# Kernel optimization log

Hardware: AMD Instinct MI355X
Metric: run time of the kernel (lower is better)

Reference implementation:

```python
import jax, jax.numpy as jnp
import numpy as np

N, L, D = 16, 128, 128
H, C = 8, 16
EPS = 1e-5


def setup_inputs() -> dict:
    key = jax.random.key(0)
    ks = jax.random.split(key, 10)
    s = 0.02
    return {
        "z": jax.random.normal(ks[0], (N, L, L, D), dtype=jnp.float32),
        "ln_w": jnp.ones((D,), jnp.float32),
        "ln_b": jnp.zeros((D,), jnp.float32),
        "Wq": jax.random.normal(ks[1], (D, H * C), jnp.float32) * s,
        "Wk": jax.random.normal(ks[2], (D, H * C), jnp.float32) * s,
        "Wv": jax.random.normal(ks[3], (D, H * C), jnp.float32) * s,
        "Wg": jax.random.normal(ks[4], (D, H * C), jnp.float32) * s,
        "bg": jnp.zeros((H * C,), jnp.float32),
        "Wo": jax.random.normal(ks[5], (H * C, D), jnp.float32) * s,
        "bo": jnp.zeros((D,), jnp.float32),
    }


def reference(z, ln_w, ln_b, Wq, Wk, Wv, Wg, bg, Wo, bo):
    n, l, _, d = z.shape
    # LayerNorm over channel dim
    mu = jnp.mean(z, axis=-1, keepdims=True)
    var = jnp.var(z, axis=-1, keepdims=True)
    zn = (z - mu) * jax.lax.rsqrt(var + EPS) * ln_w + ln_b
    # projections -> (N, L, L, H, C)
    q = (zn @ Wq).reshape(n, l, l, H, C)
    k = (zn @ Wk).reshape(n, l, l, H, C)
    v = (zn @ Wv).reshape(n, l, l, H, C)
    g = jax.nn.sigmoid(zn @ Wg + bg).reshape(n, l, l, H, C)
    # attention over the sample axis N, per pair position (a,b) and head h
    att = jnp.einsum('iabhc,jabhc->ijabh', q, k) * (1.0 / np.sqrt(C))
    att = jax.nn.softmax(att, axis=1)
    o = jnp.einsum('ijabh,jabhc->iabhc', att, v) * g
    out = o.reshape(n, l, l, H * C) @ Wo + bo
    return out
```

## Files before the change

### kernel.cpp

```cpp
#include <hip/hip_runtime.h>
#include <hip/hip_bf16.h>


typedef short bf16x8 __attribute__((ext_vector_type(8)));
typedef float f32x4 __attribute__((ext_vector_type(4)));

#define MFMA16x32(A, B, C) __builtin_amdgcn_mfma_f32_16x16x32_bf16((A), (B), (C), 0, 0, 0)

__device__ __forceinline__ unsigned short f2bf(float f) {
    unsigned int u = __float_as_uint(f);
    u += 0x7fffu + ((u >> 16) & 1u);
    return (unsigned short)(u >> 16);
}

template <int CTRL>
__device__ __forceinline__ float dpp_mov16(float x) {
    return __int_as_float(__builtin_amdgcn_update_dpp(
        0, __float_as_int(x), CTRL, 0xf, 0xf, true));
}
__device__ __forceinline__ float red16_sum(float x) {
    x += dpp_mov16<0xB1>(x);
    x += dpp_mov16<0x4E>(x);
    x += dpp_mov16<0x141>(x);
    x += dpp_mov16<0x140>(x);
    return x;
}
__device__ __forceinline__ float red16_max(float x) {
    x = fmaxf(x, dpp_mov16<0xB1>(x));
    x = fmaxf(x, dpp_mov16<0x4E>(x));
    x = fmaxf(x, dpp_mov16<0x141>(x));
    x = fmaxf(x, dpp_mov16<0x140>(x));
    return x;
}

static constexpr int  DD     = 128;
static constexpr int  NPOS   = 128 * 128;
static constexpr long ZSTR   = (long)NPOS * DD;
static constexpr int  ZN_STR = 136;
static constexpr int  SB_STR = 56;

__launch_bounds__(256, 2)
__global__ void ssattn_fused(const float* __restrict__ z,
                             const float* __restrict__ ln_w,
                             const float* __restrict__ ln_b,
                             const float* __restrict__ Wq,
                             const float* __restrict__ Wk,
                             const float* __restrict__ Wv,
                             const float* __restrict__ Wg,
                             const float* __restrict__ bg,
                             const float* __restrict__ Wo,
                             const float* __restrict__ bo,
                             float* __restrict__ out)
{
    __shared__ __align__(16) unsigned short zn_s[16 * ZN_STR];
    __shared__ __align__(16) unsigned short ob_s[16 * ZN_STR];
    __shared__ __align__(16) unsigned short qb_s[4][16 * SB_STR];
    __shared__ __align__(16) unsigned short kq_s[4][16 * SB_STR];
    __shared__ __align__(16) unsigned short vb_s[4][16 * SB_STR];
    __shared__ float lnw_s[DD];
    __shared__ float lnb_s[DD];

    const int tid  = threadIdx.x;
    const int wid  = tid >> 6;
    const int lane = tid & 63;
    const int quad = lane >> 4;
    const int lm   = lane & 15;
    const int r16  = tid >> 4;
    const int s16  = tid & 15;

    if (tid < DD) { lnw_s[tid] = ln_w[tid]; lnb_s[tid] = ln_b[tid]; }
    for (int i = tid; i < 16 * SB_STR; i += 256) {
        qb_s[0][i] = 0; qb_s[1][i] = 0; qb_s[2][i] = 0; qb_s[3][i] = 0;
        kq_s[0][i] = 0; kq_s[1][i] = 0; kq_s[2][i] = 0; kq_s[3][i] = 0;
        vb_s[0][i] = 0; vb_s[1][i] = 0; vb_s[2][i] = 0; vb_s[3][i] = 0;
    }

    bf16x8 wq_r[2][4], wk_r[2][4], wv_r[2][4], wg_r[2][4], wo_r[2][4];
    float bg_r[2], bo_r[2];
#pragma unroll
    for (int hl = 0; hl < 2; ++hl) {
        const int col = (wid * 2 + hl) * 16 + lm;
        bg_r[hl] = bg[col];
        bo_r[hl] = bo[col];
#pragma unroll
        for (int kb = 0; kb < 4; ++kb) {
            const int kbase = kb * 32 + quad * 8;
            bf16x8 a, b, c, d, e;
#pragma unroll
            for (int j = 0; j < 8; ++j) {
                const int k = kbase + j;
                a[j] = (short)f2bf(Wq[k * DD + col]);
                b[j] = (short)f2bf(Wk[k * DD + col]);
                c[j] = (short)f2bf(Wv[k * DD + col]);
                d[j] = (short)f2bf(Wg[k * DD + col]);
                e[j] = (short)f2bf(Wo[k * DD + col]);
            }
            wq_r[hl][kb] = a; wk_r[hl][kb] = b; wv_r[hl][kb] = c;
            wg_r[hl][kb] = d; wo_r[hl][kb] = e;
        }
    }
    __syncthreads();

    unsigned short* const qb = qb_s[wid];
    unsigned short* const kq = kq_s[wid];
    unsigned short* const vb = vb_s[wid];

    int p = blockIdx.x;
    float4 cura, curb;
    {
        const float* zp = z + (long)r16 * ZSTR + (long)p * DD + s16 * 8;
        cura = *(const float4*)zp;
        curb = *(const float4*)(zp + 4);
    }

    for (; p < NPOS; p += gridDim.x) {
        {
            float x[8] = {cura.x, cura.y, cura.z, cura.w, curb.x, curb.y, curb.z, curb.w};
            float s = 0.f, ss = 0.f;
#pragma unroll
            for (int j = 0; j < 8; ++j) { s += x[j]; ss += x[j] * x[j]; }
            s  = red16_sum(s);
            ss = red16_sum(ss);
            const float mu = s * (1.f / 128.f);
            const float rs = rsqrtf(ss * (1.f / 128.f) - mu * mu + 1e-5f);
            unsigned int pk[4];
#pragma unroll
            for (int jj = 0; jj < 4; ++jj) {
                const int c0 = s16 * 8 + jj * 2;
                const unsigned short lo = f2bf((x[jj * 2]     - mu) * rs * lnw_s[c0]     + lnb_s[c0]);
                const unsigned short hi = f2bf((x[jj * 2 + 1] - mu) * rs * lnw_s[c0 + 1] + lnb_s[c0 + 1]);
                pk[jj] = (unsigned)lo | ((unsigned)hi << 16);
            }
            uint4 st; st.x = pk[0]; st.y = pk[1]; st.z = pk[2]; st.w = pk[3];
            *(uint4*)&zn_s[r16 * ZN_STR + s16 * 8] = st;
        }
        __syncthreads();

        {
            const int pn  = p + gridDim.x;
            const int pnc = (pn < NPOS) ? pn : p;
            const float* zp2 = z + (long)r16 * ZSTR + (long)pnc * DD + s16 * 8;
            cura = *(const float4*)zp2;
            curb = *(const float4*)(zp2 + 4);
        }

        bf16x8 af[4];
#pragma unroll
        for (int kb = 0; kb < 4; ++kb)
            af[kb] = *(const bf16x8*)&zn_s[lm * ZN_STR + kb * 32 + quad * 8];

#pragma unroll
        for (int hl = 0; hl < 2; ++hl) {
            f32x4 aq = {0,0,0,0}, ak = {0,0,0,0}, av = {0,0,0,0}, ag = {0,0,0,0};
#pragma unroll
            for (int kb = 0; kb < 4; ++kb) {
                aq = MFMA16x32(af[kb], wq_r[hl][kb], aq);
                ak = MFMA16x32(af[kb], wk_r[hl][kb], ak);
                av = MFMA16x32(af[kb], wv_r[hl][kb], av);
                ag = MFMA16x32(af[kb], wg_r[hl][kb], ag);
            }
#pragma unroll
            for (int r = 0; r < 4; ++r) {
                const int row = quad * 4 + r;
                qb[row * SB_STR + lm] = f2bf(aq[r] * 0.25f);
                kq[row * SB_STR + lm] = f2bf(ak[r]);
                vb[lm * SB_STR + row] = f2bf(av[r]);
            }
            float gv[4];
#pragma unroll
            for (int r = 0; r < 4; ++r)
                gv[r] = 1.f / (1.f + __expf(-(ag[r] + bg_r[hl])));

            const bf16x8 aqf = *(const bf16x8*)&qb[lm * SB_STR + quad * 8];
            const bf16x8 bkf = *(const bf16x8*)&kq[lm * SB_STR + quad * 8];
            const f32x4 z4 = {0,0,0,0};
            f32x4 att = MFMA16x32(aqf, bkf, z4);

            f32x4 pr;
#pragma unroll
            for (int r = 0; r < 4; ++r) {
                const float a  = att[r];
                const float mx = red16_max(a);
                const float ex = __expf(a - mx);
                const float sm = red16_sum(ex);
                pr[r] = ex / sm;
            }
#pragma unroll
            for (int r = 0; r < 4; ++r)
                qb[(quad * 4 + r) * SB_STR + lm] = f2bf(pr[r]);

            const bf16x8 apf = *(const bf16x8*)&qb[lm * SB_STR + quad * 8];
            const bf16x8 bvf = *(const bf16x8*)&vb[lm * SB_STR + quad * 8];
            f32x4 oc = MFMA16x32(apf, bvf, z4);

            const int hcol = (wid * 2 + hl) * 16 + lm;
#pragma unroll
            for (int r = 0; r < 4; ++r)
                ob_s[(quad * 4 + r) * ZN_STR + hcol] = f2bf(oc[r] * gv[r]);
        }
        __syncthreads();

        bf16x8 of[4];
#pragma unroll
        for (int kb = 0; kb < 4; ++kb)
            of[kb] = *(const bf16x8*)&ob_s[lm * ZN_STR + kb * 32 + quad * 8];
        float* const op0 = out + (long)p * DD + (long)(quad * 4) * ZSTR;
#pragma unroll
        for (int hl = 0; hl < 2; ++hl) {
            f32x4 acc = {0,0,0,0};
#pragma unroll
            for (int kb = 0; kb < 4; ++kb)
                acc = MFMA16x32(of[kb], wo_r[hl][kb], acc);
            const int col = (wid * 2 + hl) * 16 + lm;
#pragma unroll
            for (int r = 0; r < 4; ++r)
                op0[(long)r * ZSTR + col] = acc[r] + bo_r[hl];
        }
    }
}

extern "C" void kernel_launch(void* const* d_in, const int* in_sizes, int n_in,
                              void* d_out, int out_size, void* d_ws, size_t ws_size,
                              hipStream_t stream) {
    (void)in_sizes; (void)n_in; (void)out_size; (void)d_ws; (void)ws_size;
    ssattn_fused<<<dim3(512), dim3(256), 0, stream>>>(
        (const float*)d_in[0],
        (const float*)d_in[1],
        (const float*)d_in[2],
        (const float*)d_in[3],
        (const float*)d_in[4],
        (const float*)d_in[5],
        (const float*)d_in[6],
        (const float*)d_in[7],
        (const float*)d_in[8],
        (const float*)d_in[9],
        (float*)d_out);
}
```

Before: 294.7 us.

## Process two pair positions per loop iteration and fold softmax/gate normalization

Each block iteration now handles two adjacent (a,b) positions with double-sized LDS buffers. This halves the barriers per position and doubles the prefetched z loads in flight. The 1/sqrt(C) scale is folded into Wq at load time, and the softmax normalisation and sigmoid gate are merged into a single reciprocal applied after the PV MFMA. The cost is more LDS and more registers, which could pressure the two-blocks-per-CU occupancy target.

```diff
diff --git a/kernel.cpp b/kernel.cpp
--- a/kernel.cpp
+++ b/kernel.cpp
@@ -35,6 +35,7 @@
 
 static constexpr int  DD     = 128;
 static constexpr int  NPOS   = 128 * 128;
+static constexpr int  NPAIR  = NPOS / 2;
 static constexpr long ZSTR   = (long)NPOS * DD;
 static constexpr int  ZN_STR = 136;
 static constexpr int  SB_STR = 56;
@@ -52,11 +53,11 @@
                              const float* __restrict__ bo,
                              float* __restrict__ out)
 {
-    __shared__ __align__(16) unsigned short zn_s[16 * ZN_STR];
-    __shared__ __align__(16) unsigned short ob_s[16 * ZN_STR];
-    __shared__ __align__(16) unsigned short qb_s[4][16 * SB_STR];
-    __shared__ __align__(16) unsigned short kq_s[4][16 * SB_STR];
-    __shared__ __align__(16) unsigned short vb_s[4][16 * SB_STR];
+    __shared__ __align__(16) unsigned short zn_s[2][16 * ZN_STR];
+    __shared__ __align__(16) unsigned short ob_s[2][16 * ZN_STR];
+    __shared__ __align__(16) unsigned short qb_s[4][2][16 * SB_STR];
+    __shared__ __align__(16) unsigned short kq_s[4][2][16 * SB_STR];
+    __shared__ __align__(16) unsigned short vb_s[4][2][16 * SB_STR];
     __shared__ float lnw_s[DD];
     __shared__ float lnb_s[DD];
 
@@ -69,10 +70,10 @@
     const int s16  = tid & 15;
 
     if (tid < DD) { lnw_s[tid] = ln_w[tid]; lnb_s[tid] = ln_b[tid]; }
-    for (int i = tid; i < 16 * SB_STR; i += 256) {
-        qb_s[0][i] = 0; qb_s[1][i] = 0; qb_s[2][i] = 0; qb_s[3][i] = 0;
-        kq_s[0][i] = 0; kq_s[1][i] = 0; kq_s[2][i] = 0; kq_s[3][i] = 0;
-        vb_s[0][i] = 0; vb_s[1][i] = 0; vb_s[2][i] = 0; vb_s[3][i] = 0;
+    for (int i = tid; i < 4 * 2 * 16 * SB_STR; i += 256) {
+        ((unsigned short*)qb_s)[i] = 0;
+        ((unsigned short*)kq_s)[i] = 0;
+        ((unsigned short*)vb_s)[i] = 0;
     }
 
     bf16x8 wq_r[2][4], wk_r[2][4], wv_r[2][4], wg_r[2][4], wo_r[2][4];
@@ -89,7 +90,7 @@
 #pragma unroll
             for (int j = 0; j < 8; ++j) {
                 const int k = kbase + j;
-                a[j] = (short)f2bf(Wq[k * DD + col]);
+                a[j] = (short)f2bf(Wq[k * DD + col] * 0.25f);
                 b[j] = (short)f2bf(Wk[k * DD + col]);
                 c[j] = (short)f2bf(Wv[k * DD + col]);
                 d[j] = (short)f2bf(Wg[k * DD + col]);
@@ -101,21 +102,21 @@
     }
     __syncthreads();
 
-    unsigned short* const qb = qb_s[wid];
-    unsigned short* const kq = kq_s[wid];
-    unsigned short* const vb = vb_s[wid];
-
-    int p = blockIdx.x;
-    float4 cura, curb;
+    int idx = blockIdx.x;
+    float4 cA[2], cB[2];
     {
-        const float* zp = z + (long)r16 * ZSTR + (long)p * DD + s16 * 8;
-        cura = *(const float4*)zp;
-        curb = *(const float4*)(zp + 4);
-    }
-
-    for (; p < NPOS; p += gridDim.x) {
-        {
-            float x[8] = {cura.x, cura.y, cura.z, cura.w, curb.x, curb.y, curb.z, curb.w};
+        const float* zp = z + (long)r16 * ZSTR + (long)(2 * idx) * DD + s16 * 8;
+        cA[0] = *(const float4*)zp;        cB[0] = *(const float4*)(zp + 4);
+        cA[1] = *(const float4*)(zp + DD); cB[1] = *(const float4*)(zp + DD + 4);
+    }
+
+    for (; idx < NPAIR; idx += gridDim.x) {
+        const long pbase = (long)(2 * idx) * DD;
+
+#pragma unroll
+        for (int pp = 0; pp < 2; ++pp) {
+            float x[8] = {cA[pp].x, cA[pp].y, cA[pp].z, cA[pp].w,
+                          cB[pp].x, cB[pp].y, cB[pp].z, cB[pp].w};
             float s = 0.f, ss = 0.f;
 #pragma unroll
             for (int j = 0; j < 8; ++j) { s += x[j]; ss += x[j] * x[j]; }
@@ -132,89 +133,100 @@
                 pk[jj] = (unsigned)lo | ((unsigned)hi << 16);
             }
             uint4 st; st.x = pk[0]; st.y = pk[1]; st.z = pk[2]; st.w = pk[3];
-            *(uint4*)&zn_s[r16 * ZN_STR + s16 * 8] = st;
+            *(uint4*)&zn_s[pp][r16 * ZN_STR + s16 * 8] = st;
         }
         __syncthreads();
 
         {
-            const int pn  = p + gridDim.x;
-            const int pnc = (pn < NPOS) ? pn : p;
-            const float* zp2 = z + (long)r16 * ZSTR + (long)pnc * DD + s16 * 8;
-            cura = *(const float4*)zp2;
-            curb = *(const float4*)(zp2 + 4);
-        }
-
-        bf16x8 af[4];
-#pragma unroll
-        for (int kb = 0; kb < 4; ++kb)
-            af[kb] = *(const bf16x8*)&zn_s[lm * ZN_STR + kb * 32 + quad * 8];
-
-#pragma unroll
-        for (int hl = 0; hl < 2; ++hl) {
-            f32x4 aq = {0,0,0,0}, ak = {0,0,0,0}, av = {0,0,0,0}, ag = {0,0,0,0};
-#pragma unroll
-            for (int kb = 0; kb < 4; ++kb) {
-                aq = MFMA16x32(af[kb], wq_r[hl][kb], aq);
-                ak = MFMA16x32(af[kb], wk_r[hl][kb], ak);
-                av = MFMA16x32(af[kb], wv_r[hl][kb], av);
-                ag = MFMA16x32(af[kb], wg_r[hl][kb], ag);
-            }
-#pragma unroll
-            for (int r = 0; r < 4; ++r) {
-                const int row = quad * 4 + r;
-                qb[row * SB_STR + lm] = f2bf(aq[r] * 0.25f);
-                kq[row * SB_STR + lm] = f2bf(ak[r]);
-                vb[lm * SB_STR + row] = f2bf(av[r]);
-            }
-            float gv[4];
-#pragma unroll
-            for (int r = 0; r < 4; ++r)
-                gv[r] = 1.f / (1.f + __expf(-(ag[r] + bg_r[hl])));
-
-            const bf16x8 aqf = *(const bf16x8*)&qb[lm * SB_STR + quad * 8];
-            const bf16x8 bkf = *(const bf16x8*)&kq[lm * SB_STR + quad * 8];
-            const f32x4 z4 = {0,0,0,0};
-            f32x4 att = MFMA16x32(aqf, bkf, z4);
-
-            f32x4 pr;
-#pragma unroll
-            for (int r = 0; r < 4; ++r) {
-                const float a  = att[r];
-                const float mx = red16_max(a);
-                const float ex = __expf(a - mx);
-                const float sm = red16_sum(ex);
-                pr[r] = ex / sm;
-            }
-#pragma unroll
-            for (int r = 0; r < 4; ++r)
-                qb[(quad * 4 + r) * SB_STR + lm] = f2bf(pr[r]);
-
-            const bf16x8 apf = *(const bf16x8*)&qb[lm * SB_STR + quad * 8];
-            const bf16x8 bvf = *(const bf16x8*)&vb[lm * SB_STR + quad * 8];
-            f32x4 oc = MFMA16x32(apf, bvf, z4);
-
-            const int hcol = (wid * 2 + hl) * 16 + lm;
-#pragma unroll
-            for (int r = 0; r < 4; ++r)
-                ob_s[(quad * 4 + r) * ZN_STR + hcol] = f2bf(oc[r] * gv[r]);
+            const int ni = idx + gridDim.x;
+            const int nc = (ni < NPAIR) ? ni : idx;
+            const float* zp2 = z + (long)r16 * ZSTR + (long)(2 * nc) * DD + s16 * 8;
+            cA[0] = *(const float4*)zp2;        cB[0] = *(const float4*)(zp2 + 4);
+            cA[1] = *(const float4*)(zp2 + DD); cB[1] = *(const float4*)(zp2 + DD + 4);
+        }
+
+#pragma unroll
+        for (int pp = 0; pp < 2; ++pp) {
+            unsigned short* const qbp = qb_s[wid][pp];
+            unsigned short* const kqp = kq_s[wid][pp];
+            unsigned short* const vbp = vb_s[wid][pp];
+
+            bf16x8 af[4];
+#pragma unroll
+            for (int kb = 0; kb < 4; ++kb)
+                af[kb] = *(const bf16x8*)&zn_s[pp][lm * ZN_STR + kb * 32 + quad * 8];
+
+#pragma unroll
+            for (int hl = 0; hl < 2; ++hl) {
+                f32x4 aq = {0,0,0,0}, ak = {0,0,0,0}, av = {0,0,0,0}, ag = {0,0,0,0};
+#pragma unroll
+                for (int kb = 0; kb < 4; ++kb) {
+                    aq = MFMA16x32(af[kb], wq_r[hl][kb], aq);
+                    ak = MFMA16x32(af[kb], wk_r[hl][kb], ak);
+                    av = MFMA16x32(af[kb], wv_r[hl][kb], av);
+                    ag = MFMA16x32(af[kb], wg_r[hl][kb], ag);
+                }
+#pragma unroll
+                for (int r = 0; r < 4; ++r) {
+                    const int row = quad * 4 + r;
+                    qbp[row * SB_STR + lm] = f2bf(aq[r]);
+                    kqp[row * SB_STR + lm] = f2bf(ak[r]);
+                    vbp[lm * SB_STR + row] = f2bf(av[r]);
+                }
+                float eg[4];
+#pragma unroll
+                for (int r = 0; r < 4; ++r)
+                    eg[r] = __expf(-(ag[r] + bg_r[hl]));
+
+                const bf16x8 aqf = *(const bf16x8*)&qbp[lm * SB_STR + quad * 8];
+                const bf16x8 bkf = *(const bf16x8*)&kqp[lm * SB_STR + quad * 8];
+                const f32x4 z4 = {0,0,0,0};
+                f32x4 att = MFMA16x32(aqf, bkf, z4);
+
+                f32x4 ex;
+#pragma unroll
+                for (int r = 0; r < 4; ++r) {
+                    const float mx = red16_max(att[r]);
+                    ex[r] = __expf(att[r] - mx);
+                    qbp[(quad * 4 + r) * SB_STR + lm] = f2bf(ex[r]);
+                }
+                float sc[4];
+#pragma unroll
+                for (int r = 0; r < 4; ++r) {
+                    const float sm = red16_sum(ex[r]);
+                    sc[r] = 1.f / ((1.f + eg[r]) * sm);
+                }
+
+                const bf16x8 apf = *(const bf16x8*)&qbp[lm * SB_STR + quad * 8];
+                const bf16x8 bvf = *(const bf16x8*)&vbp[lm * SB_STR + quad * 8];
+                f32x4 oc = MFMA16x32(apf, bvf, z4);
+
+                const int hcol = (wid * 2 + hl) * 16 + lm;
+#pragma unroll
+                for (int r = 0; r < 4; ++r)
+                    ob_s[pp][(quad * 4 + r) * ZN_STR + hcol] = f2bf(oc[r] * sc[r]);
+            }
         }
         __syncthreads();
 
-        bf16x8 of[4];
-#pragma unroll
-        for (int kb = 0; kb < 4; ++kb)
-            of[kb] = *(const bf16x8*)&ob_s[lm * ZN_STR + kb * 32 + quad * 8];
-        float* const op0 = out + (long)p * DD + (long)(quad * 4) * ZSTR;
-#pragma unroll
-        for (int hl = 0; hl < 2; ++hl) {
-            f32x4 acc = {0,0,0,0};
+#pragma unroll
+        for (int pp = 0; pp < 2; ++pp) {
+            bf16x8 of[4];
 #pragma unroll
             for (int kb = 0; kb < 4; ++kb)
-                acc = MFMA16x32(of[kb], wo_r[hl][kb], acc);
-            const int col = (wid * 2 + hl) * 16 + lm;
-#pragma unroll
-            for (int r = 0; r < 4; ++r)
-                op0[(long)r * ZSTR + col] = acc[r] + bo_r[hl];
+                of[kb] = *(const bf16x8*)&ob_s[pp][lm * ZN_STR + kb * 32 + quad * 8];
+            float* const op0 = out + pbase + pp * DD + (long)(quad * 4) * ZSTR;
+#pragma unroll
+            for (int hl = 0; hl < 2; ++hl) {
+                f32x4 acc = {0,0,0,0};
+#pragma unroll
+                for (int kb = 0; kb < 4; ++kb)
+                    acc = MFMA16x32(of[kb], wo_r[hl][kb], acc);
+                const int col = (wid * 2 + hl) * 16 + lm;
+#pragma unroll
+                for (int r = 0; r < 4; ++r)
+                    op0[(long)r * ZSTR + col] = acc[r] + bo_r[hl];
+            }
         }
     }
 }
```

Result: no change. 293.8 us (-0.3%).
